# Kernel optimization log

Measured on AMD Instinct MI355X. Metric: run time of the kernel, lower is better.

The kernel has to match this reference:

```python
import jax, jax.numpy as jnp
import numpy as np

N = 51200      # total nodes
G = 256        # graphs in batch
NPG = 200      # nodes per graph
E = 409600     # intra-graph edges
EPG = E // G
F_IN, HID, HEADS, NCLS = 768, 128, 4, 2


def setup_inputs() -> dict:
    key = jax.random.key(0)
    ks = jax.random.split(key, 20)
    x = jax.random.normal(ks[0], (N, F_IN), jnp.float32)
    # edges strictly inside each graph, no self-loops (PyG batching semantics)
    gid = jnp.arange(E, dtype=jnp.int32) // EPG
    sl = jax.random.randint(ks[1], (E,), 0, NPG, dtype=jnp.int32)
    off = jax.random.randint(ks[2], (E,), 1, NPG, dtype=jnp.int32)
    dl = (sl + off) % NPG
    edge_index = jnp.stack([gid * NPG + sl, gid * NPG + dl])
    batch = jnp.arange(N, dtype=jnp.int32) // NPG

    def glorot(k, shape, fan_in):
        return jax.random.normal(k, shape, jnp.float32) * np.float32(1.0 / np.sqrt(fan_in))

    return {
        'x': x, 'edge_index': edge_index, 'batch': batch,
        'W1': glorot(ks[3], (F_IN, HEADS * HID), F_IN),
        'a_src1': glorot(ks[4], (HEADS, HID), HID),
        'a_dst1': glorot(ks[5], (HEADS, HID), HID),
        'b1': jnp.zeros((HEADS * HID,), jnp.float32),
        'W2': glorot(ks[6], (HEADS * HID, HID), HEADS * HID),
        'a_src2': glorot(ks[7], (1, HID), HID),
        'a_dst2': glorot(ks[8], (1, HID), HID),
        'b2': jnp.zeros((HID,), jnp.float32),
        'Wc': glorot(ks[9], (HID, 2), HID),
        'bc': jnp.zeros((2,), jnp.float32),
        'Wf1': glorot(ks[10], (HID, HID), HID),
        'bf1': jnp.zeros((HID,), jnp.float32),
        'Wf2': glorot(ks[11], (HID, NCLS), HID),
        'bf2': jnp.zeros((NCLS,), jnp.float32),
    }


def _segment_softmax(logits, seg, num):
    m = jax.ops.segment_max(logits, seg, num_segments=num)
    e = jnp.exp(logits - m[seg])
    s = jax.ops.segment_sum(e, seg, num_segments=num)
    return e / (s[seg] + 1e-16)


def _gat(x, src, dst, W, a_s, a_d, b, n):
    # PyG GATConv, eval mode (attention dropout off), self-loops already in src/dst
    H, C = a_s.shape
    h = (x @ W).reshape(n, H, C)                       # [n,H,C]
    a_src = (h * a_s).sum(-1)                          # [n,H]
    a_dst = (h * a_d).sum(-1)
    logits = jax.nn.leaky_relu(a_src[src] + a_dst[dst], 0.2)  # [Etot,H]
    alpha = _segment_softmax(logits, dst, n)
    out = jax.ops.segment_sum(h[src] * alpha[:, :, None], dst, num_segments=n)
    return out.reshape(n, H * C) + b


def reference(x, edge_index, batch, W1, a_src1, a_dst1, b1, W2, a_src2, a_dst2, b2,
              Wc, bc, Wf1, bf1, Wf2, bf2):
    src0, dst0 = edge_index[0], edge_index[1]
    loop = jnp.arange(N, dtype=src0.dtype)
    src = jnp.concatenate([src0, loop])
    dst = jnp.concatenate([dst0, loop])

    h1 = jax.nn.relu(_gat(x, src, dst, W1, a_src1, a_dst1, b1, N))     # [N,512]
    h2 = jax.nn.relu(_gat(h1, src, dst, W2, a_src2, a_dst2, b2, N))    # [N,128]

    S = jax.nn.softmax(h2 @ Wc + bc, axis=1)                           # [N,2]

    # aggregate(): per-graph S^T A S via per-edge outer products (A from original edges)
    eg = batch[src0]
    outer = S[src0][:, :, None] * S[dst0][:, None, :]                  # [E,2,2]
    agg = jax.ops.segment_sum(outer, eg, num_segments=G)               # [G,2,2]
    rnorm = jnp.clip(jnp.abs(agg).sum(axis=2, keepdims=True), 1e-5, None)  # F.normalize p=1 dim=1
    nadj = agg / rnorm
    diag = jnp.diagonal(nadj, axis1=1, axis2=2)                        # [G,2]
    aggregate_loss = jnp.mean(jnp.mean((diag - 1.0) ** 2, axis=1))     # MSE vs ones, averaged over graphs

    # subgraph embedding: first row of S_g^T x_g per graph
    sub = jax.ops.segment_sum(S[:, 0:1] * h2, batch, num_segments=G)   # [G,128]

    out = jax.nn.relu(sub @ Wf1 + bf1)                                 # eval: dropout off
    out = out @ Wf2 + bf2                                              # [G,2]
    return out, aggregate_loss
```

## Files before the change

### kernel.cpp

```cpp
#include <hip/hip_runtime.h>
#include <hip/hip_bf16.h>
#include <cstdint>

#define N_NODES 51200
#define N_GRAPH 256
#define NPG     200
#define N_EDGE  409600
#define EPG     1600
#define F_IN    768
#define HID     128
#define HEADS   4
#define HC      512

typedef __attribute__((ext_vector_type(8))) short short8;
typedef __attribute__((ext_vector_type(4))) float floatx4;

constexpr size_t OFF_H1B    = 0;
constexpr size_t OFF_H2B    = OFF_H1B + (size_t)N_NODES * HC * 2;
constexpr size_t OFF_H2F    = OFF_H2B + (size_t)N_NODES * HID * 2;
constexpr size_t OFF_WT1    = OFF_H2F + (size_t)N_NODES * HID * 4;
constexpr size_t OFF_WT2    = OFF_WT1 + (size_t)HC * F_IN * 2;
constexpr size_t OFF_S      = OFF_WT2 + (size_t)HID * HC * 2;
constexpr size_t OFF_AGG    = OFF_S + (size_t)N_NODES * 2 * 4;
constexpr size_t OFF_SUB    = OFF_AGG + (size_t)N_GRAPH * 4 * 4;

__device__ __forceinline__ float leaky(float x) { return x >= 0.0f ? x : 0.2f * x; }

__device__ __forceinline__ unsigned short f2bf(float f) {
    unsigned int u = __float_as_uint(f);
    u += 0x7fffu + ((u >> 16) & 1u);
    return (unsigned short)(u >> 16);
}
__device__ __forceinline__ float bflo(int p) { return __uint_as_float((unsigned)p << 16); }
__device__ __forceinline__ float bfhi(int p) { return __uint_as_float((unsigned)p & 0xffff0000u); }

__device__ __forceinline__ unsigned int cvtpk(float lo, float hi) {
    unsigned int r;
    asm("v_cvt_pk_bf16_f32 %0, %1, %2" : "=v"(r) : "v"(lo), "v"(hi));
    return r;
}

__device__ __forceinline__ void gl_lds16(const void* g, void* l) {
    __builtin_amdgcn_global_load_lds(
        (__attribute__((address_space(1))) void*)(g),
        (__attribute__((address_space(3))) void*)(l),
        16, 0, 0);
}

__device__ __forceinline__ void store_cvt(short* dst, float4 a, float4 b, float4 c, float4 d) {
    uint4 q0, q1;
    q0.x = cvtpk(a.x, a.y); q0.y = cvtpk(a.z, a.w);
    q0.z = cvtpk(b.x, b.y); q0.w = cvtpk(b.z, b.w);
    q1.x = cvtpk(c.x, c.y); q1.y = cvtpk(c.z, c.w);
    q1.z = cvtpk(d.x, d.y); q1.w = cvtpk(d.z, d.w);
    *(uint4*)dst = q0;
    *(uint4*)(dst + 128) = q1;
}

__global__ __launch_bounds__(256)
void transpose_cvt_kernel(const float* __restrict__ W, short* __restrict__ Wt,
                          int K, int Nn)
{
    int idx = blockIdx.x * 256 + threadIdx.x;
    if (idx >= K * Nn) return;
    int k = idx / Nn, n = idx % Nn;
    Wt[(size_t)n * K + k] = (short)f2bf(W[idx]);
}

template <bool A_BF16>
__global__ __launch_bounds__(256)
void gemm_mfma_kernel(const void* __restrict__ Av, const short* __restrict__ Bt,
                      unsigned short* __restrict__ C, int M, int Nn, int K)
{
    __shared__ __align__(16) short Ablob[2][4096];
    __shared__ __align__(16) short Bblob[2][4096];
    const int tid = threadIdx.x;
    const int w = tid >> 6, l = tid & 63;

    const int nwg = gridDim.x;
    int wg = blockIdx.x;
    wg = (wg & 7) * (nwg >> 3) + (wg >> 3);
    const int nbx = Nn >> 7;
    const int m0 = (wg / nbx) * 128;
    const int n0 = (wg % nbx) * 128;
    const int wr = w >> 1, wc = w & 1;

    floatx4 acc[4][4];
#pragma unroll
    for (int i = 0; i < 4; ++i)
#pragma unroll
        for (int j = 0; j < 4; ++j) acc[i][j] = (floatx4)0.0f;

    const short* bgp = Bt + (size_t)(n0 + (w * 2) * 16 + (l & 15)) * K + ((l >> 4) * 8);

    const float* Af = (const float*)Av;
    const short* Ab = (const short*)Av;
    const int r = tid >> 1, hh = tid & 1;
    const float* arow = Af + (size_t)(m0 + r) * K + hh * 16;
    const short* agp = Ab + (size_t)(m0 + (w * 2) * 16 + (l & 15)) * K + ((l >> 4) * 8);
    const int oA = (r >> 4) * 512 + (2 * hh) * 128 + (r & 15) * 8;

    const int nt = K >> 5;

    if constexpr (A_BF16) {
        gl_lds16(agp,            &Ablob[0][(w * 2) * 512]);
        gl_lds16(agp + 16 * K,   &Ablob[0][(w * 2 + 1) * 512]);
    }
    gl_lds16(bgp,            &Bblob[0][(w * 2) * 512]);
    gl_lds16(bgp + 16 * K,   &Bblob[0][(w * 2 + 1) * 512]);

    float4 pA0 = {}, pA1 = {}, pA2 = {}, pA3 = {};
    float4 pB0 = {}, pB1 = {}, pB2 = {}, pB3 = {};
    if constexpr (!A_BF16) {
        float4 c0 = *(const float4*)(arow + 0);
        float4 c1 = *(const float4*)(arow + 4);
        float4 c2 = *(const float4*)(arow + 8);
        float4 c3 = *(const float4*)(arow + 12);
        store_cvt(&Ablob[0][oA], c0, c1, c2, c3);
        if (nt > 1) {
            pA0 = *(const float4*)(arow + 32);
            pA1 = *(const float4*)(arow + 36);
            pA2 = *(const float4*)(arow + 40);
            pA3 = *(const float4*)(arow + 44);
        }
    }
    __syncthreads();

    for (int t = 0; t < nt; ++t) {
        const int cur = t & 1, nxt = cur ^ 1;
        const int kn = (t + 1) << 5;

        if (t + 1 < nt) {
            gl_lds16(bgp + kn,            &Bblob[nxt][(w * 2) * 512]);
            gl_lds16(bgp + 16 * K + kn,   &Bblob[nxt][(w * 2 + 1) * 512]);
            if constexpr (A_BF16) {
                gl_lds16(agp + kn,          &Ablob[nxt][(w * 2) * 512]);
                gl_lds16(agp + 16 * K + kn, &Ablob[nxt][(w * 2 + 1) * 512]);
            }
        }
        if constexpr (!A_BF16) {
            if (t + 2 < nt) {
                const float* ap = arow + ((t + 2) << 5);
                pB0 = *(const float4*)(ap + 0);
                pB1 = *(const float4*)(ap + 4);
                pB2 = *(const float4*)(ap + 8);
                pB3 = *(const float4*)(ap + 12);
            }
        }

        short8 af[4], bfr[4];
#pragma unroll
        for (int mi = 0; mi < 4; ++mi)
            af[mi] = *(const short8*)&Ablob[cur][(wr * 4 + mi) * 512 + l * 8];
#pragma unroll
        for (int ni = 0; ni < 4; ++ni)
            bfr[ni] = *(const short8*)&Bblob[cur][(wc * 4 + ni) * 512 + l * 8];
#pragma unroll
        for (int mi = 0; mi < 4; ++mi)
#pragma unroll
            for (int ni = 0; ni < 4; ++ni)
                acc[mi][ni] = __builtin_amdgcn_mfma_f32_16x16x32_bf16(
                    af[mi], bfr[ni], acc[mi][ni], 0, 0, 0);

        if constexpr (!A_BF16) {
            if (t + 1 < nt) {
                store_cvt(&Ablob[nxt][oA], pA0, pA1, pA2, pA3);
            }
            if (t + 2 < nt) {
                pA0 = pB0; pA1 = pB1; pA2 = pB2; pA3 = pB3;
            }
        }
        __syncthreads();
    }

    const int lr = (l >> 4) * 4, lc = l & 15;
#pragma unroll
    for (int mi = 0; mi < 4; ++mi)
#pragma unroll
        for (int ni = 0; ni < 4; ++ni) {
            const size_t base = (size_t)(m0 + wr * 64 + mi * 16 + lr) * Nn
                              + (n0 + wc * 64 + ni * 16 + lc);
#pragma unroll
            for (int rr = 0; rr < 4; ++rr)
                C[base + (size_t)rr * Nn] = f2bf(acc[mi][ni][rr]);
        }
}

__global__ __launch_bounds__(512)
void gat1_kernel(const unsigned short* __restrict__ H, const int* __restrict__ src0,
                 const int* __restrict__ dst0, const float* __restrict__ a_s,
                 const float* __restrict__ a_d, const float* __restrict__ b1,
                 unsigned short* __restrict__ out)
{
    const int g = blockIdx.x, h = blockIdx.y;
    __shared__ int   s_feat[NPG * 64];
    __shared__ float s_as[NPG], s_ad[NPG], s_m[NPG], s_inv[NPG];
    __shared__ int   s_row[NPG + 1];
    __shared__ int   s_cnt[NPG];
    __shared__ int   s_scan[256];
    __shared__ unsigned short s_eraw[EPG];
    __shared__ int2  s_wc[EPG];
    const int tid = threadIdx.x, w = tid >> 6, l = tid & 63;
    const int gbase = g * NPG;

    for (int flat = tid; flat < NPG * 16; flat += 512) {
        int row = flat >> 4, q = flat & 15;
        uint4 v = *(const uint4*)(H + (size_t)(gbase + row) * HC + h * HID + q * 8);
        *(uint4*)&s_feat[row * 64 + q * 4] = v;
    }
    for (int j = tid; j < EPG; j += 512) {
        int s = src0[g * EPG + j] - gbase;
        int d = dst0[g * EPG + j] - gbase;
        s_eraw[j] = (unsigned short)(s | (d << 8));
    }
    if (tid < NPG) s_cnt[tid] = 0;
    __syncthreads();

    for (int j = tid; j < EPG; j += 512)
        atomicAdd(&s_cnt[s_eraw[j] >> 8], 1);
    const float2 av = ((const float2*)(a_s + h * HID))[l];
    const float2 dv = ((const float2*)(a_d + h * HID))[l];
    for (int nl = w; nl < NPG; nl += 8) {
        int pk = s_feat[nl * 64 + l];
        float f0 = bflo(pk), f1 = bfhi(pk);
        float ss = f0 * av.x + f1 * av.y;
        float sd = f0 * dv.x + f1 * dv.y;
#pragma unroll
        for (int off = 1; off < 64; off <<= 1) {
            ss += __shfl_xor(ss, off);
            sd += __shfl_xor(sd, off);
        }
        if (l == 0) { s_as[nl] = ss; s_ad[nl] = sd; }
    }
    __syncthreads();

    {
        int v = (tid < NPG) ? s_cnt[tid] : 0;
        if (tid < 256) s_scan[tid] = v;
        __syncthreads();
        for (int off = 1; off < 256; off <<= 1) {
            int u = (tid >= off && tid < 256) ? s_scan[tid - off] : 0;
            __syncthreads();
            if (tid < 256) s_scan[tid] += u;
            __syncthreads();
        }
        if (tid < NPG) s_row[tid + 1] = s_scan[tid];
        if (tid == 0) s_row[0] = 0;
        __syncthreads();
        if (tid < NPG) s_scan[tid] = s_row[tid];
    }
    __syncthreads();

    for (int j = tid; j < EPG; j += 512) {
        int pk = s_eraw[j];
        int p = atomicAdd(&s_scan[pk >> 8], 1);
        s_wc[p].y = pk;
    }
    __syncthreads();

    for (int j = tid; j < EPG; j += 512) {
        int pk = s_wc[j].y;
        s_wc[j].x = __float_as_int(leaky(s_as[pk & 255] + s_ad[pk >> 8]));
    }
    __syncthreads();

    if (tid < NPG) {
        float m = leaky(s_as[tid] + s_ad[tid]);
        int r0 = s_row[tid], r1 = s_row[tid + 1];
        for (int j = r0; j < r1; ++j) m = fmaxf(m, __int_as_float(s_wc[j].x));
        s_m[tid] = m;
    }
    __syncthreads();

    for (int j = tid; j < EPG; j += 512) {
        int2 e = s_wc[j];
        s_wc[j].x = __float_as_int(__expf(__int_as_float(e.x) - s_m[e.y >> 8]));
    }
    __syncthreads();

    if (tid < NPG) {
        float rs = __expf(leaky(s_as[tid] + s_ad[tid]) - s_m[tid]);
        int r0 = s_row[tid], r1 = s_row[tid + 1];
        for (int j = r0; j < r1; ++j) rs += __int_as_float(s_wc[j].x);
        s_inv[tid] = 1.0f / (rs + 1e-16f);
    }
    __syncthreads();

    const float2 bv = ((const float2*)(b1 + h * HID))[l];
    for (int nl = w; nl < NPG; nl += 8) {
        const int r0 = s_row[nl], r1 = s_row[nl + 1];
        const float wself = __expf(leaky(s_as[nl] + s_ad[nl]) - s_m[nl]);
        int spk = s_feat[nl * 64 + l];
        float a0 = wself * bflo(spk), a1 = wself * bfhi(spk);
        float c0 = 0.0f, c1 = 0.0f;
        int j = r0;
        for (; j + 4 <= r1; j += 4) {
            int2 e0 = s_wc[j], e1 = s_wc[j + 1], e2 = s_wc[j + 2], e3 = s_wc[j + 3];
            int p0 = s_feat[(e0.y & 255) * 64 + l];
            int p1 = s_feat[(e1.y & 255) * 64 + l];
            int p2 = s_feat[(e2.y & 255) * 64 + l];
            int p3 = s_feat[(e3.y & 255) * 64 + l];
            float w0 = __int_as_float(e0.x), w1 = __int_as_float(e1.x);
            float w2 = __int_as_float(e2.x), w3 = __int_as_float(e3.x);
            a0 += w0 * bflo(p0); a1 += w0 * bfhi(p0);
            c0 += w1 * bflo(p1); c1 += w1 * bfhi(p1);
            a0 += w2 * bflo(p2); a1 += w2 * bfhi(p2);
            c0 += w3 * bflo(p3); c1 += w3 * bfhi(p3);
        }
        for (; j < r1; ++j) {
            int2 e0 = s_wc[j];
            int p0 = s_feat[(e0.y & 255) * 64 + l];
            float w0 = __int_as_float(e0.x);
            a0 += w0 * bflo(p0); a1 += w0 * bfhi(p0);
        }
        const float inv = s_inv[nl];
        float o0 = (a0 + c0) * inv + bv.x;
        float o1 = (a1 + c1) * inv + bv.y;
        unsigned int st = (unsigned int)f2bf(fmaxf(o0, 0.0f))
                        | ((unsigned int)f2bf(fmaxf(o1, 0.0f)) << 16);
        *(unsigned int*)&out[(size_t)(gbase + nl) * HC + h * HID + 2 * l] = st;
    }
}

__global__ __launch_bounds__(512)
void gat2_kernel(const unsigned short* __restrict__ H, const int* __restrict__ src0,
                 const int* __restrict__ dst0, const float* __restrict__ a_s,
                 const float* __restrict__ a_d, const float* __restrict__ b2,
                 const float* __restrict__ Wc, const float* __restrict__ bc,
                 float* __restrict__ h2, float* __restrict__ S)
{
    const int g = blockIdx.x;
    __shared__ int   s_feat[NPG * 64];
    __shared__ float s_as[NPG], s_ad[NPG], s_m[NPG], s_inv[NPG];
    __shared__ int   s_row[NPG + 1];
    __shared__ int   s_cnt[NPG];
    __shared__ int   s_scan[256];
    __shared__ unsigned short s_eraw[EPG];
    __shared__ int2  s_wc[EPG];
    const int tid = threadIdx.x, w = tid >> 6, l = tid & 63;
    const int gbase = g * NPG;

    for (int flat = tid; flat < NPG * 16; flat += 512) {
        int row = flat >> 4, q = flat & 15;
        uint4 v = *(const uint4*)(H + (size_t)(gbase + row) * HID + q * 8);
        *(uint4*)&s_feat[row * 64 + q * 4] = v;
    }
    for (int j = tid; j < EPG; j += 512) {
        int s = src0[g * EPG + j] - gbase;
        int d = dst0[g * EPG + j] - gbase;
        s_eraw[j] = (unsigned short)(s | (d << 8));
    }
    if (tid < NPG) s_cnt[tid] = 0;
    __syncthreads();

    for (int j = tid; j < EPG; j += 512)
        atomicAdd(&s_cnt[s_eraw[j] >> 8], 1);
    const float2 av = ((const float2*)a_s)[l];
    const float2 dv = ((const float2*)a_d)[l];
    for (int nl = w; nl < NPG; nl += 8) {
        int pk = s_feat[nl * 64 + l];
        float f0 = bflo(pk), f1 = bfhi(pk);
        float ss = f0 * av.x + f1 * av.y;
        float sd = f0 * dv.x + f1 * dv.y;
#pragma unroll
        for (int off = 1; off < 64; off <<= 1) {
            ss += __shfl_xor(ss, off);
            sd += __shfl_xor(sd, off);
        }
        if (l == 0) { s_as[nl] = ss; s_ad[nl] = sd; }
    }
    __syncthreads();

    {
        int v = (tid < NPG) ? s_cnt[tid] : 0;
        if (tid < 256) s_scan[tid] = v;
        __syncthreads();
        for (int off = 1; off < 256; off <<= 1) {
            int u = (tid >= off && tid < 256) ? s_scan[tid - off] : 0;
            __syncthreads();
            if (tid < 256) s_scan[tid] += u;
            __syncthreads();
        }
        if (tid < NPG) s_row[tid + 1] = s_scan[tid];
        if (tid == 0) s_row[0] = 0;
        __syncthreads();
        if (tid < NPG) s_scan[tid] = s_row[tid];
    }
    __syncthreads();

    for (int j = tid; j < EPG; j += 512) {
        int pk = s_eraw[j];
        int p = atomicAdd(&s_scan[pk >> 8], 1);
        s_wc[p].y = pk;
    }
    __syncthreads();

    for (int j = tid; j < EPG; j += 512) {
        int pk = s_wc[j].y;
        s_wc[j].x = __float_as_int(leaky(s_as[pk & 255] + s_ad[pk >> 8]));
    }
    __syncthreads();

    if (tid < NPG) {
        float m = leaky(s_as[tid] + s_ad[tid]);
        int r0 = s_row[tid], r1 = s_row[tid + 1];
        for (int j = r0; j < r1; ++j) m = fmaxf(m, __int_as_float(s_wc[j].x));
        s_m[tid] = m;
    }
    __syncthreads();

    for (int j = tid; j < EPG; j += 512) {
        int2 e = s_wc[j];
        s_wc[j].x = __float_as_int(__expf(__int_as_float(e.x) - s_m[e.y >> 8]));
    }
    __syncthreads();

    if (tid < NPG) {
        float rs = __expf(leaky(s_as[tid] + s_ad[tid]) - s_m[tid]);
        int r0 = s_row[tid], r1 = s_row[tid + 1];
        for (int j = r0; j < r1; ++j) rs += __int_as_float(s_wc[j].x);
        s_inv[tid] = 1.0f / (rs + 1e-16f);
    }
    __syncthreads();

    const float2 bv = ((const float2*)b2)[l];
    const float4 wcv = ((const float4*)Wc)[l];
    const float bc0 = bc[0], bc1 = bc[1];
    for (int nl = w; nl < NPG; nl += 8) {
        const int r0 = s_row[nl], r1 = s_row[nl + 1];
        const float wself = __expf(leaky(s_as[nl] + s_ad[nl]) - s_m[nl]);
        int spk = s_feat[nl * 64 + l];
        float a0 = wself * bflo(spk), a1 = wself * bfhi(spk);
        float c0 = 0.0f, c1 = 0.0f;
        int j = r0;
        for (; j + 4 <= r1; j += 4) {
            int2 e0 = s_wc[j], e1 = s_wc[j + 1], e2 = s_wc[j + 2], e3 = s_wc[j + 3];
            int p0 = s_feat[(e0.y & 255) * 64 + l];
            int p1 = s_feat[(e1.y & 255) * 64 + l];
            int p2 = s_feat[(e2.y & 255) * 64 + l];
            int p3 = s_feat[(e3.y & 255) * 64 + l];
            float w0 = __int_as_float(e0.x), w1 = __int_as_float(e1.x);
            float w2 = __int_as_float(e2.x), w3 = __int_as_float(e3.x);
            a0 += w0 * bflo(p0); a1 += w0 * bfhi(p0);
            c0 += w1 * bflo(p1); c1 += w1 * bfhi(p1);
            a0 += w2 * bflo(p2); a1 += w2 * bfhi(p2);
            c0 += w3 * bflo(p3); c1 += w3 * bfhi(p3);
        }
        for (; j < r1; ++j) {
            int2 e0 = s_wc[j];
            int p0 = s_feat[(e0.y & 255) * 64 + l];
            float w0 = __int_as_float(e0.x);
            a0 += w0 * bflo(p0); a1 += w0 * bfhi(p0);
        }
        const float inv = s_inv[nl];
        float o0 = fmaxf((a0 + c0) * inv + bv.x, 0.0f);
        float o1 = fmaxf((a1 + c1) * inv + bv.y, 0.0f);
        *(float2*)&h2[(size_t)(gbase + nl) * HID + 2 * l] = make_float2(o0, o1);
        float z0 = o0 * wcv.x + o1 * wcv.z;
        float z1 = o0 * wcv.y + o1 * wcv.w;
#pragma unroll
        for (int off = 1; off < 64; off <<= 1) {
            z0 += __shfl_xor(z0, off);
            z1 += __shfl_xor(z1, off);
        }
        if (l == 0) {
            z0 += bc0; z1 += bc1;
            float mm = fmaxf(z0, z1);
            float e0 = __expf(z0 - mm), e1 = __expf(z1 - mm);
            float is = 1.0f / (e0 + e1);
            *(float2*)&S[(size_t)(gbase + nl) * 2] = make_float2(e0 * is, e1 * is);
        }
    }
}

__global__ __launch_bounds__(256)
void agg_kernel(const int* __restrict__ src0, const int* __restrict__ dst0,
                const float* __restrict__ S, float* __restrict__ agg)
{
    const int g = blockIdx.x, tid = threadIdx.x;
    float a00 = 0, a01 = 0, a10 = 0, a11 = 0;
    for (int e = g*EPG + tid; e < (g + 1)*EPG; e += 256) {
        int s = src0[e], d = dst0[e];
        float s0 = S[s*2], s1 = S[s*2 + 1];
        float d0 = S[d*2], d1 = S[d*2 + 1];
        a00 += s0*d0; a01 += s0*d1; a10 += s1*d0; a11 += s1*d1;
    }
    for (int off = 32; off > 0; off >>= 1) {
        a00 += __shfl_down(a00, off); a01 += __shfl_down(a01, off);
        a10 += __shfl_down(a10, off); a11 += __shfl_down(a11, off);
    }
    __shared__ float sred[4][4];
    if ((tid & 63) == 0) {
        int w = tid >> 6;
        sred[w][0] = a00; sred[w][1] = a01; sred[w][2] = a10; sred[w][3] = a11;
    }
    __syncthreads();
    if (tid == 0) {
        agg[g*4 + 0] = sred[0][0] + sred[1][0] + sred[2][0] + sred[3][0];
        agg[g*4 + 1] = sred[0][1] + sred[1][1] + sred[2][1] + sred[3][1];
        agg[g*4 + 2] = sred[0][2] + sred[1][2] + sred[2][2] + sred[3][2];
        agg[g*4 + 3] = sred[0][3] + sred[1][3] + sred[2][3] + sred[3][3];
    }
}

__global__ __launch_bounds__(256)
void loss_kernel(const float* __restrict__ agg, float* __restrict__ out_loss)
{
    int tid = threadIdx.x;
    float a00 = agg[tid*4 + 0], a01 = agg[tid*4 + 1];
    float a10 = agg[tid*4 + 2], a11 = agg[tid*4 + 3];
    float rn0 = fmaxf(fabsf(a00) + fabsf(a01), 1e-5f);
    float rn1 = fmaxf(fabsf(a10) + fabsf(a11), 1e-5f);
    float d0 = a00 / rn0 - 1.0f, d1 = a11 / rn1 - 1.0f;
    float contrib = 0.5f * (d0*d0 + d1*d1);
    for (int off = 32; off > 0; off >>= 1) contrib += __shfl_down(contrib, off);
    __shared__ float sred[4];
    if ((tid & 63) == 0) sred[tid >> 6] = contrib;
    __syncthreads();
    if (tid == 0)
        out_loss[0] = (sred[0] + sred[1] + sred[2] + sred[3]) * (1.0f / N_GRAPH);
}

__global__ __launch_bounds__(128)
void sub_kernel(const float* __restrict__ S, const float* __restrict__ h2,
                float* __restrict__ sub)
{
    const int g = blockIdx.x, c = threadIdx.x;
    const float* Sg = S + (size_t)g * NPG * 2;
    const float* hg = h2 + (size_t)g * NPG * HID;
    float acc = 0.0f;
    for (int i = 0; i < NPG; ++i)
        acc += Sg[i*2] * hg[(size_t)i*HID + c];
    sub[g*HID + c] = acc;
}

__global__ __launch_bounds__(128)
void final_kernel(const float* __restrict__ sub, const float* __restrict__ Wf1,
                  const float* __restrict__ bf1, const float* __restrict__ Wf2,
                  const float* __restrict__ bf2, float* __restrict__ out)
{
    __shared__ float s_sub[128];
    __shared__ float s_fc[128];
    const int g = blockIdx.x, t = threadIdx.x;
    s_sub[t] = sub[g*HID + t];
    __syncthreads();
    float acc = bf1[t];
    for (int c = 0; c < 128; ++c)
        acc += s_sub[c] * Wf1[c*128 + t];
    s_fc[t] = fmaxf(acc, 0.0f);
    __syncthreads();
    if (t < 2) {
        float z = bf2[t];
        for (int j = 0; j < 128; ++j) z += s_fc[j] * Wf2[j*2 + t];
        out[g*2 + t] = z;
    }
}

extern "C" void kernel_launch(void* const* d_in, const int* in_sizes, int n_in,
                              void* d_out, int out_size, void* d_ws, size_t ws_size,
                              hipStream_t stream)
{
    const float* x   = (const float*)d_in[0];
    const int*   ei  = (const int*)d_in[1];
    const float* W1  = (const float*)d_in[3];
    const float* as1 = (const float*)d_in[4];
    const float* ad1 = (const float*)d_in[5];
    const float* b1  = (const float*)d_in[6];
    const float* W2  = (const float*)d_in[7];
    const float* as2 = (const float*)d_in[8];
    const float* ad2 = (const float*)d_in[9];
    const float* b2  = (const float*)d_in[10];
    const float* Wc  = (const float*)d_in[11];
    const float* bc  = (const float*)d_in[12];
    const float* Wf1 = (const float*)d_in[13];
    const float* bf1 = (const float*)d_in[14];
    const float* Wf2 = (const float*)d_in[15];
    const float* bf2 = (const float*)d_in[16];
    const int* src0 = ei;
    const int* dst0 = ei + N_EDGE;

    char* ws = (char*)d_ws;
    unsigned short* H1b = (unsigned short*)(ws + OFF_H1B);
    unsigned short* H2b = (unsigned short*)(ws + OFF_H2B);
    float* h2    = (float*)(ws + OFF_H2F);
    short* Wt1   = (short*)(ws + OFF_WT1);
    short* Wt2   = (short*)(ws + OFF_WT2);
    float* Sbuf  = (float*)(ws + OFF_S);
    float* aggb  = (float*)(ws + OFF_AGG);
    float* subb  = (float*)(ws + OFF_SUB);
    float* out   = (float*)d_out;

    transpose_cvt_kernel<<<(F_IN*HC + 255)/256, 256, 0, stream>>>(W1, Wt1, F_IN, HC);
    transpose_cvt_kernel<<<(HC*HID + 255)/256, 256, 0, stream>>>(W2, Wt2, HC, HID);

    gemm_mfma_kernel<false><<<(N_NODES/128) * (HC/128), 256, 0, stream>>>(
        x, Wt1, H1b, N_NODES, HC, F_IN);

    gat1_kernel<<<dim3(N_GRAPH, HEADS), 512, 0, stream>>>(
        H1b, src0, dst0, as1, ad1, b1, H1b);

    gemm_mfma_kernel<true><<<(N_NODES/128) * (HID/128), 256, 0, stream>>>(
        H1b, Wt2, H2b, N_NODES, HID, HC);

    gat2_kernel<<<N_GRAPH, 512, 0, stream>>>(
        H2b, src0, dst0, as2, ad2, b2, Wc, bc, h2, Sbuf);

    agg_kernel<<<N_GRAPH, 256, 0, stream>>>(src0, dst0, Sbuf, aggb);
    loss_kernel<<<1, 256, 0, stream>>>(aggb, out + N_GRAPH*2);

    sub_kernel<<<N_GRAPH, 128, 0, stream>>>(Sbuf, h2, subb);
    final_kernel<<<N_GRAPH, 128, 0, stream>>>(subb, Wf1, bf1, Wf2, bf2, out);

    (void)in_sizes; (void)n_in; (void)out_size; (void)ws_size;
}
```

Baseline: 498.0 us.

## Deepen GEMM pipeline to triple-buffered LDS with explicit waitcnt barriers

Restructures the MFMA GEMM main loop so B (and A in the bf16 path) uses three LDS buffers with a prefetch distance of two k-tiles. The fp32-A path keeps three register stages rotated through a 3x-unrolled macro. __syncthreads is replaced by explicit s_waitcnt vmcnt/lgkmcnt counts plus s_barrier, so later loads can stay in flight across the barrier. This aims to hide more global-load latency, at the cost of extra LDS and registers, which may lower occupancy. It also relies on hand-counted vmcnt values being correct.

```diff
diff --git a/kernel.cpp b/kernel.cpp
--- a/kernel.cpp
+++ b/kernel.cpp
@@ -72,8 +72,8 @@
 void gemm_mfma_kernel(const void* __restrict__ Av, const short* __restrict__ Bt,
                       unsigned short* __restrict__ C, int M, int Nn, int K)
 {
-    __shared__ __align__(16) short Ablob[2][4096];
-    __shared__ __align__(16) short Bblob[2][4096];
+    __shared__ __align__(16) short Bblob[3][4096];
+    __shared__ __align__(16) short Ablob[A_BF16 ? 3 : 2][4096];
     const int tid = threadIdx.x;
     const int w = tid >> 6, l = tid & 63;
 
@@ -84,6 +84,7 @@
     const int m0 = (wg / nbx) * 128;
     const int n0 = (wg % nbx) * 128;
     const int wr = w >> 1, wc = w & 1;
+    const int wofs = w * 1024;
 
     floatx4 acc[4][4];
 #pragma unroll
@@ -92,85 +93,112 @@
         for (int j = 0; j < 4; ++j) acc[i][j] = (floatx4)0.0f;
 
     const short* bgp = Bt + (size_t)(n0 + (w * 2) * 16 + (l & 15)) * K + ((l >> 4) * 8);
-
-    const float* Af = (const float*)Av;
-    const short* Ab = (const short*)Av;
-    const int r = tid >> 1, hh = tid & 1;
-    const float* arow = Af + (size_t)(m0 + r) * K + hh * 16;
-    const short* agp = Ab + (size_t)(m0 + (w * 2) * 16 + (l & 15)) * K + ((l >> 4) * 8);
-    const int oA = (r >> 4) * 512 + (2 * hh) * 128 + (r & 15) * 8;
-
     const int nt = K >> 5;
 
-    if constexpr (A_BF16) {
-        gl_lds16(agp,            &Ablob[0][(w * 2) * 512]);
-        gl_lds16(agp + 16 * K,   &Ablob[0][(w * 2 + 1) * 512]);
-    }
-    gl_lds16(bgp,            &Bblob[0][(w * 2) * 512]);
-    gl_lds16(bgp + 16 * K,   &Bblob[0][(w * 2 + 1) * 512]);
-
-    float4 pA0 = {}, pA1 = {}, pA2 = {}, pA3 = {};
-    float4 pB0 = {}, pB1 = {}, pB2 = {}, pB3 = {};
-    if constexpr (!A_BF16) {
-        float4 c0 = *(const float4*)(arow + 0);
-        float4 c1 = *(const float4*)(arow + 4);
-        float4 c2 = *(const float4*)(arow + 8);
-        float4 c3 = *(const float4*)(arow + 12);
-        store_cvt(&Ablob[0][oA], c0, c1, c2, c3);
-        if (nt > 1) {
-            pA0 = *(const float4*)(arow + 32);
-            pA1 = *(const float4*)(arow + 36);
-            pA2 = *(const float4*)(arow + 40);
-            pA3 = *(const float4*)(arow + 44);
-        }
-    }
-    __syncthreads();
-
-    for (int t = 0; t < nt; ++t) {
-        const int cur = t & 1, nxt = cur ^ 1;
-        const int kn = (t + 1) << 5;
-
-        if (t + 1 < nt) {
-            gl_lds16(bgp + kn,            &Bblob[nxt][(w * 2) * 512]);
-            gl_lds16(bgp + 16 * K + kn,   &Bblob[nxt][(w * 2 + 1) * 512]);
-            if constexpr (A_BF16) {
-                gl_lds16(agp + kn,          &Ablob[nxt][(w * 2) * 512]);
-                gl_lds16(agp + 16 * K + kn, &Ablob[nxt][(w * 2 + 1) * 512]);
-            }
-        }
-        if constexpr (!A_BF16) {
-            if (t + 2 < nt) {
-                const float* ap = arow + ((t + 2) << 5);
-                pB0 = *(const float4*)(ap + 0);
-                pB1 = *(const float4*)(ap + 4);
-                pB2 = *(const float4*)(ap + 8);
-                pB3 = *(const float4*)(ap + 12);
-            }
-        }
-
+    auto compute = [&](int ai, int bi) {
         short8 af[4], bfr[4];
 #pragma unroll
         for (int mi = 0; mi < 4; ++mi)
-            af[mi] = *(const short8*)&Ablob[cur][(wr * 4 + mi) * 512 + l * 8];
+            af[mi] = *(const short8*)&Ablob[ai][(wr * 4 + mi) * 512 + l * 8];
 #pragma unroll
         for (int ni = 0; ni < 4; ++ni)
-            bfr[ni] = *(const short8*)&Bblob[cur][(wc * 4 + ni) * 512 + l * 8];
+            bfr[ni] = *(const short8*)&Bblob[bi][(wc * 4 + ni) * 512 + l * 8];
 #pragma unroll
         for (int mi = 0; mi < 4; ++mi)
 #pragma unroll
             for (int ni = 0; ni < 4; ++ni)
                 acc[mi][ni] = __builtin_amdgcn_mfma_f32_16x16x32_bf16(
                     af[mi], bfr[ni], acc[mi][ni], 0, 0, 0);
-
-        if constexpr (!A_BF16) {
+    };
+
+    if constexpr (A_BF16) {
+        const short* agp = (const short*)Av
+            + (size_t)(m0 + (w * 2) * 16 + (l & 15)) * K + ((l >> 4) * 8);
+        gl_lds16(agp,               &Ablob[0][wofs]);
+        gl_lds16(agp + 16 * K,      &Ablob[0][wofs + 512]);
+        gl_lds16(bgp,               &Bblob[0][wofs]);
+        gl_lds16(bgp + 16 * K,      &Bblob[0][wofs + 512]);
+        gl_lds16(agp + 32,          &Ablob[1][wofs]);
+        gl_lds16(agp + 16 * K + 32, &Ablob[1][wofs + 512]);
+        gl_lds16(bgp + 32,          &Bblob[1][wofs]);
+        gl_lds16(bgp + 16 * K + 32, &Bblob[1][wofs + 512]);
+        asm volatile("s_waitcnt vmcnt(4)" ::: "memory");
+        __builtin_amdgcn_s_barrier();
+
+        int cur3 = 0;
+        for (int t = 0; t < nt; ++t) {
+            int nn3 = cur3 + 2; if (nn3 >= 3) nn3 -= 3;
+            if (t + 2 < nt) {
+                const int kk = (t + 2) << 5;
+                gl_lds16(agp + kk,          &Ablob[nn3][wofs]);
+                gl_lds16(agp + 16 * K + kk, &Ablob[nn3][wofs + 512]);
+                gl_lds16(bgp + kk,          &Bblob[nn3][wofs]);
+                gl_lds16(bgp + 16 * K + kk, &Bblob[nn3][wofs + 512]);
+            }
+            compute(cur3, cur3);
             if (t + 1 < nt) {
-                store_cvt(&Ablob[nxt][oA], pA0, pA1, pA2, pA3);
+                if (t + 2 < nt) asm volatile("s_waitcnt vmcnt(4) lgkmcnt(0)" ::: "memory");
+                else            asm volatile("s_waitcnt vmcnt(0) lgkmcnt(0)" ::: "memory");
+                __builtin_amdgcn_s_barrier();
             }
-            if (t + 2 < nt) {
-                pA0 = pB0; pA1 = pB1; pA2 = pB2; pA3 = pB3;
-            }
-        }
-        __syncthreads();
+            cur3 += 1; if (cur3 == 3) cur3 = 0;
+        }
+    } else {
+        const float* Af = (const float*)Av;
+        const int r = tid >> 1, hh = tid & 1;
+        const float* arow = Af + (size_t)(m0 + r) * K + hh * 16;
+        const int oA = (r >> 4) * 512 + (2 * hh) * 128 + (r & 15) * 8;
+
+        float4 sa0, sa1, sa2, sa3, sb0, sb1, sb2, sb3, sc0, sc1, sc2, sc3;
+
+#define LOADA4(P0, P1, P2, P3, T) { const float* ap_ = arow + ((T) << 5); \
+        P0 = *(const float4*)(ap_ + 0); P1 = *(const float4*)(ap_ + 4);   \
+        P2 = *(const float4*)(ap_ + 8); P3 = *(const float4*)(ap_ + 12); }
+
+        gl_lds16(bgp,               &Bblob[0][wofs]);
+        gl_lds16(bgp + 16 * K,      &Bblob[0][wofs + 512]);
+        gl_lds16(bgp + 32,          &Bblob[1][wofs]);
+        gl_lds16(bgp + 16 * K + 32, &Bblob[1][wofs + 512]);
+        LOADA4(sa0, sa1, sa2, sa3, 0);
+        LOADA4(sb0, sb1, sb2, sb3, 1);
+        LOADA4(sc0, sc1, sc2, sc3, 2);
+        asm volatile("s_waitcnt vmcnt(8)" ::: "memory");
+        store_cvt(&Ablob[0][oA], sa0, sa1, sa2, sa3);
+        asm volatile("s_waitcnt lgkmcnt(0)" ::: "memory");
+        __builtin_amdgcn_s_barrier();
+
+        int cur3 = 0;
+#define GITER(T, SS0, SS1, SS2, SS3, SL0, SL1, SL2, SL3) {                      \
+        const int t_ = (T);                                                     \
+        if (t_ < nt) {                                                          \
+            int nn3 = cur3 + 2; if (nn3 >= 3) nn3 -= 3;                         \
+            if (t_ + 2 < nt) {                                                  \
+                const int kk = (t_ + 2) << 5;                                   \
+                gl_lds16(bgp + kk,          &Bblob[nn3][wofs]);                 \
+                gl_lds16(bgp + 16 * K + kk, &Bblob[nn3][wofs + 512]);           \
+            }                                                                   \
+            if (t_ + 3 < nt) LOADA4(SL0, SL1, SL2, SL3, t_ + 3);                \
+            compute(t_ & 1, cur3);                                              \
+            if (t_ + 1 < nt) {                                                  \
+                store_cvt(&Ablob[(t_ + 1) & 1][oA], SS0, SS1, SS2, SS3);        \
+                if (t_ + 3 < nt)                                                \
+                    asm volatile("s_waitcnt vmcnt(10) lgkmcnt(0)" ::: "memory");\
+                else if (t_ + 2 < nt)                                           \
+                    asm volatile("s_waitcnt vmcnt(6) lgkmcnt(0)" ::: "memory"); \
+                else                                                            \
+                    asm volatile("s_waitcnt vmcnt(0) lgkmcnt(0)" ::: "memory"); \
+                __builtin_amdgcn_s_barrier();                                   \
+            }                                                                   \
+            cur3 += 1; if (cur3 == 3) cur3 = 0;                                 \
+        } }
+
+        for (int t3 = 0; t3 < nt; t3 += 3) {
+            GITER(t3 + 0, sb0, sb1, sb2, sb3, sa0, sa1, sa2, sa3);
+            GITER(t3 + 1, sc0, sc1, sc2, sc3, sb0, sb1, sb2, sb3);
+            GITER(t3 + 2, sa0, sa1, sa2, sa3, sc0, sc1, sc2, sc3);
+        }
+#undef GITER
+#undef LOADA4
     }
 
     const int lr = (l >> 4) * 4, lc = l & 15;
```

Result: no change. 501.8 us (+0.7%).
